# Optimization experiments

Hardware: AMD Instinct MI355X
Metric: run time of the kernel (lower is better)

Reference implementation:

```python
import jax, jax.numpy as jnp
import numpy as np
from jax import lax

B, T, I, H, O = 2048, 512, 1, 64, 1


def setup_inputs() -> dict:
    key = jax.random.key(0)
    ks = jax.random.split(key, 7)
    stdv = 1.0 / np.sqrt(H)
    return {
        "x": jax.random.normal(ks[0], (B, T, I), dtype=jnp.float32),
        "w_ih": jax.random.uniform(ks[1], (4 * H, I), jnp.float32, -stdv, stdv),
        "w_hh": jax.random.uniform(ks[2], (4 * H, H), jnp.float32, -stdv, stdv),
        "b_ih": jax.random.uniform(ks[3], (4 * H,), jnp.float32, -stdv, stdv),
        "b_hh": jax.random.uniform(ks[4], (4 * H,), jnp.float32, -stdv, stdv),
        "w_fc": jax.random.uniform(ks[5], (O, H), jnp.float32, -stdv, stdv),
        "b_fc": jax.random.uniform(ks[6], (O,), jnp.float32, -stdv, stdv),
    }


def reference(x, w_ih, w_hh, b_ih, b_hh, w_fc, b_fc):
    # x: [B, T, I] (batch_first). Precompute input contribution to gates for all t.
    xT = jnp.swapaxes(x, 0, 1)                                  # [T, B, I]
    x_gates = jnp.einsum("tbi,gi->tbg", xT, w_ih) + b_ih + b_hh  # [T, B, 4H]

    def step(carry, xg):
        h, c = carry
        gates = xg + h @ w_hh.T                                  # [B, 4H]
        i, f, g, o = jnp.split(gates, 4, axis=-1)                # PyTorch gate order i,f,g,o
        i = jax.nn.sigmoid(i)
        f = jax.nn.sigmoid(f)
        g = jnp.tanh(g)
        o = jax.nn.sigmoid(o)
        c = f * c + i * g
        h = o * jnp.tanh(c)
        return (h, c), h

    h0 = jnp.zeros((x.shape[0], w_hh.shape[1]), x.dtype)
    c0 = jnp.zeros_like(h0)
    _, hs = lax.scan(step, (h0, c0), x_gates)                    # hs: [T, B, H]
    hs = jnp.swapaxes(hs, 0, 1)                                  # [B, T, H]
    return hs @ w_fc.T + b_fc                                    # [B, T, O]
```

## Files before the change

### kernel.cpp

```cpp
#include <hip/hip_runtime.h>

#define T_STEPS 512
#define HSTR 80
#define XSTRIDE 520
#define OSTRIDE 513
#define NB 4

typedef _Float16 half8v __attribute__((ext_vector_type(8)));
typedef _Float16 half4v __attribute__((ext_vector_type(4)));
typedef float f32x4 __attribute__((ext_vector_type(4)));

#define K1 1.442695041f
#define K2 2.885390082f

__device__ __forceinline__ float ex2(float x) {
#if __has_builtin(__builtin_amdgcn_exp2f)
    return __builtin_amdgcn_exp2f(x);
#else
    return exp2f(x);
#endif
}
__device__ __forceinline__ float rcp_fast(float x) {
#if __has_builtin(__builtin_amdgcn_rcpf)
    return __builtin_amdgcn_rcpf(x);
#else
    return 1.0f / x;
#endif
}

__device__ __forceinline__ float out_dot(half8v a0, half8v a1,
                                         const float* wfc0, const float* wfc1) {
    float s = 0.f;
#pragma unroll
    for (int j = 0; j < 8; ++j) s = fmaf((float)a0[j], wfc0[j], s);
#pragma unroll
    for (int j = 0; j < 8; ++j) s = fmaf((float)a1[j], wfc1[j], s);
    s += __shfl_xor(s, 16);
    s += __shfl_xor(s, 32);
    return s;
}

__global__ __launch_bounds__(256, 2) void lstm_kernel(
    const float* __restrict__ x, const float* __restrict__ w_ih,
    const float* __restrict__ w_hh, const float* __restrict__ b_ih,
    const float* __restrict__ b_hh, const float* __restrict__ w_fc,
    const float* __restrict__ b_fc, float* __restrict__ out)
{
    __shared__ __align__(16) _Float16 hbuf[2][NB * HSTR];
    __shared__ __align__(16) _Float16 xls[NB * XSTRIDE];
    __shared__ __align__(16) float ols[NB * OSTRIDE];

    const int tid  = threadIdx.x;
    const int w    = tid >> 6;
    const int lane = tid & 63;
    const int q    = lane >> 4;
    const int c    = lane & 15;
    const int bown = q;
    const int b0   = blockIdx.x * NB;

    for (int i = tid; i < NB * 128; i += 256) {
        int b  = i >> 7;
        int t4 = i & 127;
        float4 v = *(const float4*)(x + (size_t)(b0 + b) * T_STEPS + t4 * 4);
        half4v hv;
        hv[0] = (_Float16)v.x; hv[1] = (_Float16)v.y;
        hv[2] = (_Float16)v.z; hv[3] = (_Float16)v.w;
        *(half4v*)(&xls[b * XSTRIDE + t4 * 4]) = hv;
    }
    for (int i = tid; i < 2 * NB * HSTR / 2; i += 256) ((int*)hbuf)[i] = 0;

    const float sK[4] = { -K1, -K1, K2, -K1 };
    half8v bfrag[4][2];
    float biasS[4], wihS[4];
#pragma unroll
    for (int n = 0; n < 4; ++n) {
        int g = 64 * n + 16 * w + c;
        biasS[n] = (b_ih[g] + b_hh[g]) * sK[n];
        wihS[n]  = w_ih[g] * sK[n];
#pragma unroll
        for (int kk = 0; kk < 2; ++kk) {
            const float* wp = w_hh + g * 64 + 32 * kk + 8 * q;
            float4 lo  = *(const float4*)(wp);
            float4 hi4 = *(const float4*)(wp + 4);
            half8v f;
            f[0] = (_Float16)(lo.x  * sK[n]); f[1] = (_Float16)(lo.y  * sK[n]);
            f[2] = (_Float16)(lo.z  * sK[n]); f[3] = (_Float16)(lo.w  * sK[n]);
            f[4] = (_Float16)(hi4.x * sK[n]); f[5] = (_Float16)(hi4.y * sK[n]);
            f[6] = (_Float16)(hi4.z * sK[n]); f[7] = (_Float16)(hi4.w * sK[n]);
            bfrag[n][kk] = f;
        }
    }

    float wfc0[8], wfc1[8];
#pragma unroll
    for (int j = 0; j < 8; ++j) { wfc0[j] = w_fc[8 * q + j]; wfc1[j] = w_fc[32 + 8 * q + j]; }
    const float bfc = b_fc[0];

    float cs = 0.f;
    const f32x4 zeroq = {0.f, 0.f, 0.f, 0.f};

    __syncthreads();

    half8v sa0 = {}, sa1 = {};

    for (int tq = 0; tq < 128; ++tq) {
        half4v xh = *(const half4v*)(&xls[bown * XSTRIDE + tq * 4]);

#pragma unroll
        for (int dt = 0; dt < 4; ++dt) {
            const int t  = tq * 4 + dt;
            const int rb = t & 1;
            const _Float16* hrd = hbuf[rb];

            const _Float16* hp = hrd + (c >> 2) * HSTR + 8 * q;
            half8v a0 = *(const half8v*)(hp);
            half8v a1 = *(const half8v*)(hp + 32);

            if (dt == w) { sa0 = a0; sa1 = a1; }

            const float xv = (float)xh[dt];
            float xb[4];
#pragma unroll
            for (int n = 0; n < 4; ++n) xb[n] = fmaf(xv, wihS[n], biasS[n]);

            f32x4 acc[4];
#pragma unroll
            for (int n = 0; n < 4; ++n) {
                acc[n] = __builtin_amdgcn_mfma_f32_16x16x32_f16(a1, bfrag[n][1], zeroq, 0, 0, 0);
                acc[n] = __builtin_amdgcn_mfma_f32_16x16x32_f16(a0, bfrag[n][0], acc[n], 0, 0, 0);
            }

            float v4[4];
#pragma unroll
            for (int n = 0; n < 4; ++n) v4[n] = acc[n][0] + xb[n];

            _Float16* hwr = hbuf[rb ^ 1];
            {
                float A  = ex2(v4[0]);
                float Bt = ex2(v4[2]);
                float ig = (Bt - 1.0f) * rcp_fast((1.0f + A) * (1.0f + Bt));
                float rf = rcp_fast(1.0f + ex2(v4[1]));
                cs = fmaf(cs, rf, ig);
                float cc = fminf(fmaxf(cs, -15.f), 15.f);
                float Ao = ex2(v4[3]);
                float C  = ex2(cc * K2);
                float h  = (C - 1.0f) * rcp_fast((1.0f + Ao) * (1.0f + C));
                hwr[bown * HSTR + 16 * w + c] = (_Float16)h;
            }
            __syncthreads();
        }

        {
            int st = tq * 4 + w;
            if (st > 0) {
                float s = out_dot(sa0, sa1, wfc0, wfc1);
                if (lane < 16 && (lane & 3) == 0)
                    ols[(lane >> 2) * OSTRIDE + (st - 1)] = s + bfc;
            }
        }
    }

    if (w == 3) {
        const _Float16* hp = hbuf[0] + (c >> 2) * HSTR + 8 * q;
        half8v a0 = *(const half8v*)(hp);
        half8v a1 = *(const half8v*)(hp + 32);
        float s = out_dot(a0, a1, wfc0, wfc1);
        if (lane < 16 && (lane & 3) == 0)
            ols[(lane >> 2) * OSTRIDE + (T_STEPS - 1)] = s + bfc;
    }
    __syncthreads();

    for (int i = tid; i < NB * T_STEPS; i += 256) {
        int b = i >> 9;
        int t = i & (T_STEPS - 1);
        out[(size_t)(b0 + b) * T_STEPS + t] = ols[b * OSTRIDE + t];
    }
}

extern "C" void kernel_launch(void* const* d_in, const int* in_sizes, int n_in,
                              void* d_out, int out_size, void* d_ws, size_t ws_size,
                              hipStream_t stream) {
    const float* x    = (const float*)d_in[0];
    const float* w_ih = (const float*)d_in[1];
    const float* w_hh = (const float*)d_in[2];
    const float* b_ih = (const float*)d_in[3];
    const float* b_hh = (const float*)d_in[4];
    const float* w_fc = (const float*)d_in[5];
    const float* b_fc = (const float*)d_in[6];
    float* out = (float*)d_out;
    hipLaunchKernelGGL(lstm_kernel, dim3(2048 / NB), dim3(256), 0, stream,
                       x, w_ih, w_hh, b_ih, b_hh, w_fc, b_fc, out);
}
```

Baseline: 254.7 us.

## Process eight batch rows per block with two independent LSTM chains per wave

Doubles the batch rows per block from 4 to 8. Each wave now runs two independent 4-row groups (A and B) per timestep, each with its own MFMA chains, activations and cell state. This halves the grid to 256 blocks and interleaves two dependency chains to hide MFMA and transcendental latency, at the cost of doubled register and LDS use. Launch bounds drop to one block per SIMD group, so occupancy falls.

New measurement: 324.2 us. 27.3% more time.

```diff
diff --git a/kernel.cpp b/kernel.cpp
--- a/kernel.cpp
+++ b/kernel.cpp
@@ -4,7 +4,7 @@
 #define HSTR 80
 #define XSTRIDE 520
 #define OSTRIDE 513
-#define NB 4
+#define NB 8
 
 typedef _Float16 half8v __attribute__((ext_vector_type(8)));
 typedef _Float16 half4v __attribute__((ext_vector_type(4)));
@@ -28,6 +28,19 @@
 #endif
 }
 
+__device__ __forceinline__ float lstm_act(float v0, float v1, float v2, float v3,
+                                          float& cs) {
+    float A  = ex2(v0);
+    float Bt = ex2(v2);
+    float ig = (Bt - 1.0f) * rcp_fast((1.0f + A) * (1.0f + Bt));
+    float rf = rcp_fast(1.0f + ex2(v1));
+    cs = fmaf(cs, rf, ig);
+    float cc = fminf(fmaxf(cs, -15.f), 15.f);
+    float Ao = ex2(v3);
+    float C  = ex2(cc * K2);
+    return (C - 1.0f) * rcp_fast((1.0f + Ao) * (1.0f + C));
+}
+
 __device__ __forceinline__ float out_dot(half8v a0, half8v a1,
                                          const float* wfc0, const float* wfc1) {
     float s = 0.f;
@@ -40,7 +53,7 @@
     return s;
 }
 
-__global__ __launch_bounds__(256, 2) void lstm_kernel(
+__global__ __launch_bounds__(256, 1) void lstm_kernel(
     const float* __restrict__ x, const float* __restrict__ w_ih,
     const float* __restrict__ w_hh, const float* __restrict__ b_ih,
     const float* __restrict__ b_hh, const float* __restrict__ w_fc,
@@ -55,7 +68,6 @@
     const int lane = tid & 63;
     const int q    = lane >> 4;
     const int c    = lane & 15;
-    const int bown = q;
     const int b0   = blockIdx.x * NB;
 
     for (int i = tid; i < NB * 128; i += 256) {
@@ -96,15 +108,16 @@
     for (int j = 0; j < 8; ++j) { wfc0[j] = w_fc[8 * q + j]; wfc1[j] = w_fc[32 + 8 * q + j]; }
     const float bfc = b_fc[0];
 
-    float cs = 0.f;
+    float csA = 0.f, csB = 0.f;
     const f32x4 zeroq = {0.f, 0.f, 0.f, 0.f};
 
     __syncthreads();
 
-    half8v sa0 = {}, sa1 = {};
+    half8v sa0A = {}, sa1A = {}, sa0B = {}, sa1B = {};
 
     for (int tq = 0; tq < 128; ++tq) {
-        half4v xh = *(const half4v*)(&xls[bown * XSTRIDE + tq * 4]);
+        half4v xhA = *(const half4v*)(&xls[q * XSTRIDE + tq * 4]);
+        half4v xhB = *(const half4v*)(&xls[(4 + q) * XSTRIDE + tq * 4]);
 
 #pragma unroll
         for (int dt = 0; dt < 4; ++dt) {
@@ -112,61 +125,76 @@
             const int rb = t & 1;
             const _Float16* hrd = hbuf[rb];
 
-            const _Float16* hp = hrd + (c >> 2) * HSTR + 8 * q;
-            half8v a0 = *(const half8v*)(hp);
-            half8v a1 = *(const half8v*)(hp + 32);
-
-            if (dt == w) { sa0 = a0; sa1 = a1; }
-
-            const float xv = (float)xh[dt];
-            float xb[4];
-#pragma unroll
-            for (int n = 0; n < 4; ++n) xb[n] = fmaf(xv, wihS[n], biasS[n]);
-
-            f32x4 acc[4];
+            const _Float16* hpA = hrd + (c >> 2) * HSTR + 8 * q;
+            const _Float16* hpB = hrd + (4 + (c >> 2)) * HSTR + 8 * q;
+            half8v a0A = *(const half8v*)(hpA);
+            half8v a1A = *(const half8v*)(hpA + 32);
+            half8v a0B = *(const half8v*)(hpB);
+            half8v a1B = *(const half8v*)(hpB + 32);
+
+            if (dt == w) { sa0A = a0A; sa1A = a1A; sa0B = a0B; sa1B = a1B; }
+
+            const float xvA = (float)xhA[dt], xvB = (float)xhB[dt];
+            float xbA[4], xbB[4];
 #pragma unroll
             for (int n = 0; n < 4; ++n) {
-                acc[n] = __builtin_amdgcn_mfma_f32_16x16x32_f16(a1, bfrag[n][1], zeroq, 0, 0, 0);
-                acc[n] = __builtin_amdgcn_mfma_f32_16x16x32_f16(a0, bfrag[n][0], acc[n], 0, 0, 0);
-            }
-
-            float v4[4];
-#pragma unroll
-            for (int n = 0; n < 4; ++n) v4[n] = acc[n][0] + xb[n];
+                xbA[n] = fmaf(xvA, wihS[n], biasS[n]);
+                xbB[n] = fmaf(xvB, wihS[n], biasS[n]);
+            }
+
+            f32x4 accA[4], accB[4];
+#pragma unroll
+            for (int n = 0; n < 4; ++n) {
+                accA[n] = __builtin_amdgcn_mfma_f32_16x16x32_f16(a1A, bfrag[n][1], zeroq, 0, 0, 0);
+                accA[n] = __builtin_amdgcn_mfma_f32_16x16x32_f16(a0A, bfrag[n][0], accA[n], 0, 0, 0);
+            }
+#pragma unroll
+            for (int n = 0; n < 4; ++n) {
+                accB[n] = __builtin_amdgcn_mfma_f32_16x16x32_f16(a1B, bfrag[n][1], zeroq, 0, 0, 0);
+                accB[n] = __builtin_amdgcn_mfma_f32_16x16x32_f16(a0B, bfrag[n][0], accB[n], 0, 0, 0);
+            }
+
+            float vA[4], vB[4];
+#pragma unroll
+            for (int n = 0; n < 4; ++n) vA[n] = accA[n][0] + xbA[n];
+#pragma unroll
+            for (int n = 0; n < 4; ++n) vB[n] = accB[n][0] + xbB[n];
 
             _Float16* hwr = hbuf[rb ^ 1];
-            {
-                float A  = ex2(v4[0]);
-                float Bt = ex2(v4[2]);
-                float ig = (Bt - 1.0f) * rcp_fast((1.0f + A) * (1.0f + Bt));
-                float rf = rcp_fast(1.0f + ex2(v4[1]));
-                cs = fmaf(cs, rf, ig);
-                float cc = fminf(fmaxf(cs, -15.f), 15.f);
-                float Ao = ex2(v4[3]);
-                float C  = ex2(cc * K2);
-                float h  = (C - 1.0f) * rcp_fast((1.0f + Ao) * (1.0f + C));
-                hwr[bown * HSTR + 16 * w + c] = (_Float16)h;
-            }
+            float hA = lstm_act(vA[0], vA[1], vA[2], vA[3], csA);
+            hwr[q * HSTR + 16 * w + c] = (_Float16)hA;
+            float hB = lstm_act(vB[0], vB[1], vB[2], vB[3], csB);
+            hwr[(4 + q) * HSTR + 16 * w + c] = (_Float16)hB;
+
             __syncthreads();
         }
 
         {
             int st = tq * 4 + w;
             if (st > 0) {
-                float s = out_dot(sa0, sa1, wfc0, wfc1);
-                if (lane < 16 && (lane & 3) == 0)
-                    ols[(lane >> 2) * OSTRIDE + (st - 1)] = s + bfc;
+                float sA = out_dot(sa0A, sa1A, wfc0, wfc1);
+                float sB = out_dot(sa0B, sa1B, wfc0, wfc1);
+                if (lane < 16 && (lane & 3) == 0) {
+                    ols[(lane >> 2) * OSTRIDE + (st - 1)]       = sA + bfc;
+                    ols[(4 + (lane >> 2)) * OSTRIDE + (st - 1)] = sB + bfc;
+                }
             }
         }
     }
 
     if (w == 3) {
-        const _Float16* hp = hbuf[0] + (c >> 2) * HSTR + 8 * q;
-        half8v a0 = *(const half8v*)(hp);
-        half8v a1 = *(const half8v*)(hp + 32);
-        float s = out_dot(a0, a1, wfc0, wfc1);
-        if (lane < 16 && (lane & 3) == 0)
-            ols[(lane >> 2) * OSTRIDE + (T_STEPS - 1)] = s + bfc;
+        const _Float16* hpA = hbuf[0] + (c >> 2) * HSTR + 8 * q;
+        const _Float16* hpB = hbuf[0] + (4 + (c >> 2)) * HSTR + 8 * q;
+        half8v a0A = *(const half8v*)(hpA);
+        half8v a1A = *(const half8v*)(hpA + 32);
+        half8v a0B = *(const half8v*)(hpB);
+        half8v a1B = *(const half8v*)(hpB + 32);
+        float sA = out_dot(a0A, a1A, wfc0, wfc1);
+        float sB = out_dot(a0B, a1B, wfc0, wfc1);
+        if (lane < 16 && (lane & 3) == 0) {
+            ols[(lane >> 2) * OSTRIDE + (T_STEPS - 1)]       = sA + bfc;
+            ols[(4 + (lane >> 2)) * OSTRIDE + (T_STEPS - 1)] = sB + bfc;
+        }
     }
     __syncthreads();
 
```

## Halve LSTM block to two waves, each computing two hidden-unit slices per step

Applied to the files above, without the earlier changes.

Changes the per-block work split from four wavefronts, each owning 16 hidden units, to two wavefronts each owning 32 units in two 16-unit halves with separate MFMA groups and cell states. The goal is cheaper per-step barriers among fewer waves, and interleaving one half's activation math with the other half's matrix ops inside a wave. The cost is twice the serial work per wave on the recurrence critical path, more registers per thread, and fewer resident waves per CU for latency hiding. The output-projection schedule is changed to match the two-wave layout.

Result: slower. 390.7 us (+53.4%).

```diff
diff --git a/kernel.cpp b/kernel.cpp
--- a/kernel.cpp
+++ b/kernel.cpp
@@ -8,6 +8,7 @@
 
 typedef _Float16 half8v __attribute__((ext_vector_type(8)));
 typedef _Float16 half4v __attribute__((ext_vector_type(4)));
+typedef _Float16 half2v __attribute__((ext_vector_type(2)));
 typedef float f32x4 __attribute__((ext_vector_type(4)));
 
 #define K1 1.442695041f
@@ -28,6 +29,19 @@
 #endif
 }
 
+__device__ __forceinline__ float lstm_act(float v0, float v1, float v2, float v3,
+                                          float& cs) {
+    float A  = ex2(v0);
+    float Bt = ex2(v2);
+    float ig = (Bt - 1.0f) * rcp_fast((1.0f + A) * (1.0f + Bt));
+    float rf = rcp_fast(1.0f + ex2(v1));
+    cs = fmaf(cs, rf, ig);
+    float cc = fminf(fmaxf(cs, -15.f), 15.f);
+    float Ao = ex2(v3);
+    float C  = ex2(cc * K2);
+    return (C - 1.0f) * rcp_fast((1.0f + Ao) * (1.0f + C));
+}
+
 __device__ __forceinline__ float out_dot(half8v a0, half8v a1,
                                          const float* wfc0, const float* wfc1) {
     float s = 0.f;
@@ -40,7 +54,7 @@
     return s;
 }
 
-__global__ __launch_bounds__(256, 2) void lstm_kernel(
+__global__ __launch_bounds__(128, 1) void lstm_kernel(
     const float* __restrict__ x, const float* __restrict__ w_ih,
     const float* __restrict__ w_hh, const float* __restrict__ b_ih,
     const float* __restrict__ b_hh, const float* __restrict__ w_fc,
@@ -55,10 +69,9 @@
     const int lane = tid & 63;
     const int q    = lane >> 4;
     const int c    = lane & 15;
-    const int bown = q;
     const int b0   = blockIdx.x * NB;
 
-    for (int i = tid; i < NB * 128; i += 256) {
+    for (int i = tid; i < NB * 128; i += 128) {
         int b  = i >> 7;
         int t4 = i & 127;
         float4 v = *(const float4*)(x + (size_t)(b0 + b) * T_STEPS + t4 * 4);
@@ -67,27 +80,30 @@
         hv[2] = (_Float16)v.z; hv[3] = (_Float16)v.w;
         *(half4v*)(&xls[b * XSTRIDE + t4 * 4]) = hv;
     }
-    for (int i = tid; i < 2 * NB * HSTR / 2; i += 256) ((int*)hbuf)[i] = 0;
+    for (int i = tid; i < 2 * NB * HSTR / 2; i += 128) ((int*)hbuf)[i] = 0;
 
     const float sK[4] = { -K1, -K1, K2, -K1 };
-    half8v bfrag[4][2];
-    float biasS[4], wihS[4];
+    half8v bfrag[4][2][2];
+    float biasS[4][2], wihS[4][2];
 #pragma unroll
     for (int n = 0; n < 4; ++n) {
-        int g = 64 * n + 16 * w + c;
-        biasS[n] = (b_ih[g] + b_hh[g]) * sK[n];
-        wihS[n]  = w_ih[g] * sK[n];
-#pragma unroll
-        for (int kk = 0; kk < 2; ++kk) {
-            const float* wp = w_hh + g * 64 + 32 * kk + 8 * q;
-            float4 lo  = *(const float4*)(wp);
-            float4 hi4 = *(const float4*)(wp + 4);
-            half8v f;
-            f[0] = (_Float16)(lo.x  * sK[n]); f[1] = (_Float16)(lo.y  * sK[n]);
-            f[2] = (_Float16)(lo.z  * sK[n]); f[3] = (_Float16)(lo.w  * sK[n]);
-            f[4] = (_Float16)(hi4.x * sK[n]); f[5] = (_Float16)(hi4.y * sK[n]);
-            f[6] = (_Float16)(hi4.z * sK[n]); f[7] = (_Float16)(hi4.w * sK[n]);
-            bfrag[n][kk] = f;
+#pragma unroll
+        for (int ui = 0; ui < 2; ++ui) {
+            int g = 64 * n + 32 * w + 16 * ui + c;
+            biasS[n][ui] = (b_ih[g] + b_hh[g]) * sK[n];
+            wihS[n][ui]  = w_ih[g] * sK[n];
+#pragma unroll
+            for (int kk = 0; kk < 2; ++kk) {
+                const float* wp = w_hh + g * 64 + 32 * kk + 8 * q;
+                float4 lo  = *(const float4*)(wp);
+                float4 hi4 = *(const float4*)(wp + 4);
+                half8v f;
+                f[0] = (_Float16)(lo.x  * sK[n]); f[1] = (_Float16)(lo.y  * sK[n]);
+                f[2] = (_Float16)(lo.z  * sK[n]); f[3] = (_Float16)(lo.w  * sK[n]);
+                f[4] = (_Float16)(hi4.x * sK[n]); f[5] = (_Float16)(hi4.y * sK[n]);
+                f[6] = (_Float16)(hi4.z * sK[n]); f[7] = (_Float16)(hi4.w * sK[n]);
+                bfrag[n][ui][kk] = f;
+            }
         }
     }
 
@@ -96,62 +112,66 @@
     for (int j = 0; j < 8; ++j) { wfc0[j] = w_fc[8 * q + j]; wfc1[j] = w_fc[32 + 8 * q + j]; }
     const float bfc = b_fc[0];
 
-    float cs = 0.f;
+    float cs0 = 0.f, cs1 = 0.f;
     const f32x4 zeroq = {0.f, 0.f, 0.f, 0.f};
 
     __syncthreads();
 
     half8v sa0 = {}, sa1 = {};
 
-    for (int tq = 0; tq < 128; ++tq) {
-        half4v xh = *(const half4v*)(&xls[bown * XSTRIDE + tq * 4]);
-
-#pragma unroll
-        for (int dt = 0; dt < 4; ++dt) {
-            const int t  = tq * 4 + dt;
+    for (int tq = 0; tq < 256; ++tq) {
+        half2v xh = *(const half2v*)(&xls[q * XSTRIDE + 2 * tq]);
+
+#pragma unroll
+        for (int dt = 0; dt < 2; ++dt) {
+            const int t  = 2 * tq + dt;
             const int rb = t & 1;
-            const _Float16* hrd = hbuf[rb];
-
-            const _Float16* hp = hrd + (c >> 2) * HSTR + 8 * q;
+
+            const _Float16* hp = hbuf[rb] + (c >> 2) * HSTR + 8 * q;
             half8v a0 = *(const half8v*)(hp);
             half8v a1 = *(const half8v*)(hp + 32);
 
             if (dt == w) { sa0 = a0; sa1 = a1; }
 
             const float xv = (float)xh[dt];
-            float xb[4];
-#pragma unroll
-            for (int n = 0; n < 4; ++n) xb[n] = fmaf(xv, wihS[n], biasS[n]);
-
-            f32x4 acc[4];
+            float xb[4][2];
 #pragma unroll
             for (int n = 0; n < 4; ++n) {
-                acc[n] = __builtin_amdgcn_mfma_f32_16x16x32_f16(a1, bfrag[n][1], zeroq, 0, 0, 0);
-                acc[n] = __builtin_amdgcn_mfma_f32_16x16x32_f16(a0, bfrag[n][0], acc[n], 0, 0, 0);
-            }
-
-            float v4[4];
-#pragma unroll
-            for (int n = 0; n < 4; ++n) v4[n] = acc[n][0] + xb[n];
+                xb[n][0] = fmaf(xv, wihS[n][0], biasS[n][0]);
+                xb[n][1] = fmaf(xv, wihS[n][1], biasS[n][1]);
+            }
 
             _Float16* hwr = hbuf[rb ^ 1];
+
+            f32x4 acc0[4];
+#pragma unroll
+            for (int n = 0; n < 4; ++n) {
+                acc0[n] = __builtin_amdgcn_mfma_f32_16x16x32_f16(a1, bfrag[n][0][1], zeroq, 0, 0, 0);
+                acc0[n] = __builtin_amdgcn_mfma_f32_16x16x32_f16(a0, bfrag[n][0][0], acc0[n], 0, 0, 0);
+            }
             {
-                float A  = ex2(v4[0]);
-                float Bt = ex2(v4[2]);
-                float ig = (Bt - 1.0f) * rcp_fast((1.0f + A) * (1.0f + Bt));
-                float rf = rcp_fast(1.0f + ex2(v4[1]));
-                cs = fmaf(cs, rf, ig);
-                float cc = fminf(fmaxf(cs, -15.f), 15.f);
-                float Ao = ex2(v4[3]);
-                float C  = ex2(cc * K2);
-                float h  = (C - 1.0f) * rcp_fast((1.0f + Ao) * (1.0f + C));
-                hwr[bown * HSTR + 16 * w + c] = (_Float16)h;
-            }
+                float h0 = lstm_act(acc0[0][0] + xb[0][0], acc0[1][0] + xb[1][0],
+                                    acc0[2][0] + xb[2][0], acc0[3][0] + xb[3][0], cs0);
+                hwr[q * HSTR + 32 * w + c] = (_Float16)h0;
+            }
+
+            f32x4 acc1[4];
+#pragma unroll
+            for (int n = 0; n < 4; ++n) {
+                acc1[n] = __builtin_amdgcn_mfma_f32_16x16x32_f16(a1, bfrag[n][1][1], zeroq, 0, 0, 0);
+                acc1[n] = __builtin_amdgcn_mfma_f32_16x16x32_f16(a0, bfrag[n][1][0], acc1[n], 0, 0, 0);
+            }
+            {
+                float h1 = lstm_act(acc1[0][0] + xb[0][1], acc1[1][0] + xb[1][1],
+                                    acc1[2][0] + xb[2][1], acc1[3][0] + xb[3][1], cs1);
+                hwr[q * HSTR + 32 * w + 16 + c] = (_Float16)h1;
+            }
+
             __syncthreads();
         }
 
         {
-            int st = tq * 4 + w;
+            int st = 2 * tq + w;
             if (st > 0) {
                 float s = out_dot(sa0, sa1, wfc0, wfc1);
                 if (lane < 16 && (lane & 3) == 0)
@@ -160,7 +180,7 @@
         }
     }
 
-    if (w == 3) {
+    if (w == 1) {
         const _Float16* hp = hbuf[0] + (c >> 2) * HSTR + 8 * q;
         half8v a0 = *(const half8v*)(hp);
         half8v a1 = *(const half8v*)(hp + 32);
@@ -170,7 +190,7 @@
     }
     __syncthreads();
 
-    for (int i = tid; i < NB * T_STEPS; i += 256) {
+    for (int i = tid; i < NB * T_STEPS; i += 128) {
         int b = i >> 9;
         int t = i & (T_STEPS - 1);
         out[(size_t)(b0 + b) * T_STEPS + t] = ols[b * OSTRIDE + t];
@@ -188,6 +208,6 @@
     const float* w_fc = (const float*)d_in[5];
     const float* b_fc = (const float*)d_in[6];
     float* out = (float*)d_out;
-    hipLaunchKernelGGL(lstm_kernel, dim3(2048 / NB), dim3(256), 0, stream,
+    hipLaunchKernelGGL(lstm_kernel, dim3(2048 / NB), dim3(128), 0, stream,
                        x, w_ih, w_hh, b_ih, b_hh, w_fc, b_fc, out);
 }
```

## Give each wavefront its own batch pair and software-pipeline the two hidden halves

Applied to the files above, without the earlier changes.

Each wavefront now owns two batch rows and holds the full recurrent weight matrix in registers, so the per-step block-wide __syncthreads is replaced by wave-local LDS exchange with s_waitcnt. The hidden state is split into two 32-unit halves whose gate activations are staggered against the MFMAs of the other half, with sched_group_barrier hints to interleave transcendental math and matrix ops. The grid drops to 256 blocks with one block per CU, so the goal is to remove barrier latency and hide the activation chain behind MFMA work. The cost is much higher register pressure from holding 32 weight fragments per lane, plus lower occupancy.

Measured after the change: 376.4 us. 1.48x slower.

```diff
diff --git a/kernel.cpp b/kernel.cpp
--- a/kernel.cpp
+++ b/kernel.cpp
@@ -4,7 +4,6 @@
 #define HSTR 80
 #define XSTRIDE 520
 #define OSTRIDE 513
-#define NB 4
 
 typedef _Float16 half8v __attribute__((ext_vector_type(8)));
 typedef _Float16 half4v __attribute__((ext_vector_type(4)));
@@ -12,6 +11,11 @@
 
 #define K1 1.442695041f
 #define K2 2.885390082f
+#define CZCL 43.28085123f
+
+#define MFMA16(A,B,C) __builtin_amdgcn_mfma_f32_16x16x32_f16((A),(B),(C),0,0,0)
+#define SGB(m,n) __builtin_amdgcn_sched_group_barrier((m),(n),0)
+#define LGKM0 asm volatile("s_waitcnt lgkmcnt(0)" ::: "memory")
 
 __device__ __forceinline__ float ex2(float x) {
 #if __has_builtin(__builtin_amdgcn_exp2f)
@@ -28,67 +32,62 @@
 #endif
 }
 
-__device__ __forceinline__ float out_dot(half8v a0, half8v a1,
-                                         const float* wfc0, const float* wfc1) {
-    float s = 0.f;
-#pragma unroll
-    for (int j = 0; j < 8; ++j) s = fmaf((float)a0[j], wfc0[j], s);
-#pragma unroll
-    for (int j = 0; j < 8; ++j) s = fmaf((float)a1[j], wfc1[j], s);
-    s += __shfl_xor(s, 16);
-    s += __shfl_xor(s, 32);
-    return s;
-}
-
-__global__ __launch_bounds__(256, 2) void lstm_kernel(
+__global__ __launch_bounds__(256, 1) void lstm_kernel(
     const float* __restrict__ x, const float* __restrict__ w_ih,
     const float* __restrict__ w_hh, const float* __restrict__ b_ih,
     const float* __restrict__ b_hh, const float* __restrict__ w_fc,
     const float* __restrict__ b_fc, float* __restrict__ out)
 {
-    __shared__ __align__(16) _Float16 hbuf[2][NB * HSTR];
-    __shared__ __align__(16) _Float16 xls[NB * XSTRIDE];
-    __shared__ __align__(16) float ols[NB * OSTRIDE];
+    __shared__ __align__(16) _Float16 hls[4][2 * HSTR];
+    __shared__ __align__(16) _Float16 xls[8][XSTRIDE];
+    __shared__ __align__(16) float    ols[8][OSTRIDE];
 
     const int tid  = threadIdx.x;
     const int w    = tid >> 6;
     const int lane = tid & 63;
     const int q    = lane >> 4;
     const int c    = lane & 15;
-    const int bown = q;
-    const int b0   = blockIdx.x * NB;
-
-    for (int i = tid; i < NB * 128; i += 256) {
-        int b  = i >> 7;
-        int t4 = i & 127;
-        float4 v = *(const float4*)(x + (size_t)(b0 + b) * T_STEPS + t4 * 4);
+    const int up   = q & 1;
+    const int mb   = q >> 1;
+    const int bw   = blockIdx.x * 8 + 2 * w;
+
+    for (int i = lane; i < 256; i += 64) {
+        int r = i >> 7, t4 = i & 127;
+        float4 v = *(const float4*)(x + (size_t)(bw + r) * T_STEPS + t4 * 4);
         half4v hv;
         hv[0] = (_Float16)v.x; hv[1] = (_Float16)v.y;
         hv[2] = (_Float16)v.z; hv[3] = (_Float16)v.w;
-        *(half4v*)(&xls[b * XSTRIDE + t4 * 4]) = hv;
-    }
-    for (int i = tid; i < 2 * NB * HSTR / 2; i += 256) ((int*)hbuf)[i] = 0;
+        *(half4v*)(&xls[2 * w + r][t4 * 4]) = hv;
+    }
+    _Float16* hbw = &hls[w][0];
+    for (int i = lane; i < 80; i += 64) ((int*)hbw)[i] = 0;
 
     const float sK[4] = { -K1, -K1, K2, -K1 };
-    half8v bfrag[4][2];
-    float biasS[4], wihS[4];
+    half8v bfrag[4][4][2];
+    float biasA[4], wihA[4], biasB[4], wihB[4];
 #pragma unroll
     for (int n = 0; n < 4; ++n) {
-        int g = 64 * n + 16 * w + c;
-        biasS[n] = (b_ih[g] + b_hh[g]) * sK[n];
-        wihS[n]  = w_ih[g] * sK[n];
-#pragma unroll
-        for (int kk = 0; kk < 2; ++kk) {
-            const float* wp = w_hh + g * 64 + 32 * kk + 8 * q;
-            float4 lo  = *(const float4*)(wp);
-            float4 hi4 = *(const float4*)(wp + 4);
-            half8v f;
-            f[0] = (_Float16)(lo.x  * sK[n]); f[1] = (_Float16)(lo.y  * sK[n]);
-            f[2] = (_Float16)(lo.z  * sK[n]); f[3] = (_Float16)(lo.w  * sK[n]);
-            f[4] = (_Float16)(hi4.x * sK[n]); f[5] = (_Float16)(hi4.y * sK[n]);
-            f[6] = (_Float16)(hi4.z * sK[n]); f[7] = (_Float16)(hi4.w * sK[n]);
-            bfrag[n][kk] = f;
+#pragma unroll
+        for (int u = 0; u < 4; ++u) {
+            int g = 64 * n + 16 * u + c;
+#pragma unroll
+            for (int kk = 0; kk < 2; ++kk) {
+                const float* wp = w_hh + g * 64 + 32 * kk + 8 * q;
+                float4 lo  = *(const float4*)(wp);
+                float4 hi4 = *(const float4*)(wp + 4);
+                half8v f;
+                f[0] = (_Float16)(lo.x  * sK[n]); f[1] = (_Float16)(lo.y  * sK[n]);
+                f[2] = (_Float16)(lo.z  * sK[n]); f[3] = (_Float16)(lo.w  * sK[n]);
+                f[4] = (_Float16)(hi4.x * sK[n]); f[5] = (_Float16)(hi4.y * sK[n]);
+                f[6] = (_Float16)(hi4.z * sK[n]); f[7] = (_Float16)(hi4.w * sK[n]);
+                bfrag[n][u][kk] = f;
+            }
         }
+        int gA = 64 * n + 16 * up + c;
+        biasA[n] = (b_ih[gA] + b_hh[gA]) * sK[n];
+        wihA[n]  = w_ih[gA] * sK[n];
+        biasB[n] = (b_ih[gA + 32] + b_hh[gA + 32]) * sK[n];
+        wihB[n]  = w_ih[gA + 32] * sK[n];
     }
 
     float wfc0[8], wfc1[8];
@@ -96,84 +95,141 @@
     for (int j = 0; j < 8; ++j) { wfc0[j] = w_fc[8 * q + j]; wfc1[j] = w_fc[32 + 8 * q + j]; }
     const float bfc = b_fc[0];
 
-    float cs = 0.f;
+    float czA = 0.f, czB = 0.f;
+    float vB0 = 100.f, vB1 = 100.f, vB2 = 0.f, vB3 = 100.f;
     const f32x4 zeroq = {0.f, 0.f, 0.f, 0.f};
 
-    __syncthreads();
-
-    half8v sa0 = {}, sa1 = {};
+    LGKM0;
+    const _Float16* hp = hbw + (c >> 3) * HSTR + 8 * q;
+    half8v a0 = *(const half8v*)(hp);
+    half8v a1 = *(const half8v*)(hp + 32);
+
+    f32x4 acc[4][4];
 
     for (int tq = 0; tq < 128; ++tq) {
-        half4v xh = *(const half4v*)(&xls[bown * XSTRIDE + tq * 4]);
-
+        half4v xh = *(const half4v*)(&xls[2 * w + mb][tq * 4]);
 #pragma unroll
         for (int dt = 0; dt < 4; ++dt) {
             const int t  = tq * 4 + dt;
-            const int rb = t & 1;
-            const _Float16* hrd = hbuf[rb];
-
-            const _Float16* hp = hrd + (c >> 2) * HSTR + 8 * q;
-            half8v a0 = *(const half8v*)(hp);
-            half8v a1 = *(const half8v*)(hp + 32);
-
-            if (dt == w) { sa0 = a0; sa1 = a1; }
-
             const float xv = (float)xh[dt];
-            float xb[4];
-#pragma unroll
-            for (int n = 0; n < 4; ++n) xb[n] = fmaf(xv, wihS[n], biasS[n]);
-
-            f32x4 acc[4];
-#pragma unroll
-            for (int n = 0; n < 4; ++n) {
-                acc[n] = __builtin_amdgcn_mfma_f32_16x16x32_f16(a1, bfrag[n][1], zeroq, 0, 0, 0);
-                acc[n] = __builtin_amdgcn_mfma_f32_16x16x32_f16(a0, bfrag[n][0], acc[n], 0, 0, 0);
-            }
-
-            float v4[4];
-#pragma unroll
-            for (int n = 0; n < 4; ++n) v4[n] = acc[n][0] + xb[n];
-
-            _Float16* hwr = hbuf[rb ^ 1];
-            {
-                float A  = ex2(v4[0]);
-                float Bt = ex2(v4[2]);
-                float ig = (Bt - 1.0f) * rcp_fast((1.0f + A) * (1.0f + Bt));
-                float rf = rcp_fast(1.0f + ex2(v4[1]));
-                cs = fmaf(cs, rf, ig);
-                float cc = fminf(fmaxf(cs, -15.f), 15.f);
-                float Ao = ex2(v4[3]);
-                float C  = ex2(cc * K2);
-                float h  = (C - 1.0f) * rcp_fast((1.0f + Ao) * (1.0f + C));
-                hwr[bown * HSTR + 16 * w + c] = (_Float16)h;
-            }
-            __syncthreads();
+
+            acc[0][0] = MFMA16(a0, bfrag[0][0][0], zeroq);
+            acc[1][0] = MFMA16(a0, bfrag[1][0][0], zeroq);
+            float bA = ex2(vB0), bB = ex2(vB2), bF = ex2(vB1), bO = ex2(vB3);
+            SGB(8, 2); SGB(2, 4);
+            acc[2][0] = MFMA16(a0, bfrag[2][0][0], zeroq);
+            acc[3][0] = MFMA16(a0, bfrag[3][0][0], zeroq);
+            float bR  = rcp_fast((1.f + bA) * (1.f + bB));
+            float bpg = fmaf(bB, K2, -K2);
+            float brf = rcp_fast(1.f + bF);
+            SGB(8, 2); SGB(2, 6);
+            acc[0][1] = MFMA16(a0, bfrag[0][1][0], zeroq);
+            acc[1][1] = MFMA16(a0, bfrag[1][1][0], zeroq);
+            czB = fmaf(czB, brf, bpg * bR);
+            float bcc = fminf(fmaxf(czB, -CZCL), CZCL);
+            float bC  = ex2(bcc);
+            SGB(8, 2); SGB(2, 5);
+            acc[2][1] = MFMA16(a0, bfrag[2][1][0], zeroq);
+            acc[3][1] = MFMA16(a0, bfrag[3][1][0], zeroq);
+            float bh = (bC - 1.f) * rcp_fast((1.f + bO) * (1.f + bC));
+            hbw[mb * HSTR + 32 + 16 * up + c] = (_Float16)bh;
+            SGB(8, 2); SGB(2, 6);
+            LGKM0;
+            a1 = *(const half8v*)(hp + 32);
+            acc[0][2] = MFMA16(a0, bfrag[0][2][0], zeroq);
+            acc[1][2] = MFMA16(a0, bfrag[1][2][0], zeroq);
+            acc[2][2] = MFMA16(a0, bfrag[2][2][0], zeroq);
+            acc[3][2] = MFMA16(a0, bfrag[3][2][0], zeroq);
+            acc[0][3] = MFMA16(a0, bfrag[0][3][0], zeroq);
+            acc[1][3] = MFMA16(a0, bfrag[1][3][0], zeroq);
+            acc[2][3] = MFMA16(a0, bfrag[2][3][0], zeroq);
+            acc[3][3] = MFMA16(a0, bfrag[3][3][0], zeroq);
+            SGB(8, 8);
+
+            acc[0][0] = MFMA16(a1, bfrag[0][0][1], acc[0][0]);
+            acc[1][0] = MFMA16(a1, bfrag[1][0][1], acc[1][0]);
+            acc[2][0] = MFMA16(a1, bfrag[2][0][1], acc[2][0]);
+            acc[3][0] = MFMA16(a1, bfrag[3][0][1], acc[3][0]);
+            acc[0][1] = MFMA16(a1, bfrag[0][1][1], acc[0][1]);
+            acc[1][1] = MFMA16(a1, bfrag[1][1][1], acc[1][1]);
+            acc[2][1] = MFMA16(a1, bfrag[2][1][1], acc[2][1]);
+            acc[3][1] = MFMA16(a1, bfrag[3][1][1], acc[3][1]);
+            SGB(8, 8);
+            float av0 = (up ? acc[0][1][0] : acc[0][0][0]) + fmaf(xv, wihA[0], biasA[0]);
+            float av1 = (up ? acc[1][1][0] : acc[1][0][0]) + fmaf(xv, wihA[1], biasA[1]);
+            float av2 = (up ? acc[2][1][0] : acc[2][0][0]) + fmaf(xv, wihA[2], biasA[2]);
+            float av3 = (up ? acc[3][1][0] : acc[3][0][0]) + fmaf(xv, wihA[3], biasA[3]);
+            float aA = ex2(av0), aB2 = ex2(av2), aF = ex2(av1), aO = ex2(av3);
+            SGB(2, 16);
+            acc[0][2] = MFMA16(a1, bfrag[0][2][1], acc[0][2]);
+            acc[1][2] = MFMA16(a1, bfrag[1][2][1], acc[1][2]);
+            float aR  = rcp_fast((1.f + aA) * (1.f + aB2));
+            float apg = fmaf(aB2, K2, -K2);
+            float arf = rcp_fast(1.f + aF);
+            SGB(8, 2); SGB(2, 6);
+            acc[2][2] = MFMA16(a1, bfrag[2][2][1], acc[2][2]);
+            acc[3][2] = MFMA16(a1, bfrag[3][2][1], acc[3][2]);
+            czA = fmaf(czA, arf, apg * aR);
+            float acl = fminf(fmaxf(czA, -CZCL), CZCL);
+            float aC  = ex2(acl);
+            SGB(8, 2); SGB(2, 5);
+            acc[0][3] = MFMA16(a1, bfrag[0][3][1], acc[0][3]);
+            acc[1][3] = MFMA16(a1, bfrag[1][3][1], acc[1][3]);
+            float ah = (aC - 1.f) * rcp_fast((1.f + aO) * (1.f + aC));
+            hbw[mb * HSTR + 16 * up + c] = (_Float16)ah;
+            SGB(8, 2); SGB(2, 6);
+            LGKM0;
+            half8v a0n = *(const half8v*)(hp);
+            acc[2][3] = MFMA16(a1, bfrag[2][3][1], acc[2][3]);
+            acc[3][3] = MFMA16(a1, bfrag[3][3][1], acc[3][3]);
+            SGB(8, 2);
+
+            float s = 0.f;
+#pragma unroll
+            for (int j = 0; j < 8; ++j) s = fmaf((float)a0[j], wfc0[j], s);
+#pragma unroll
+            for (int j = 0; j < 8; ++j) s = fmaf((float)a1[j], wfc1[j], s);
+            s += __shfl_xor(s, 16);
+            s += __shfl_xor(s, 32);
+            if (t && (lane == 0 || lane == 8))
+                ols[2 * w + (lane >> 3)][t - 1] = s + bfc;
+
+            vB0 = (up ? acc[0][3][0] : acc[0][2][0]) + fmaf(xv, wihB[0], biasB[0]);
+            vB1 = (up ? acc[1][3][0] : acc[1][2][0]) + fmaf(xv, wihB[1], biasB[1]);
+            vB2 = (up ? acc[2][3][0] : acc[2][2][0]) + fmaf(xv, wihB[2], biasB[2]);
+            vB3 = (up ? acc[3][3][0] : acc[3][2][0]) + fmaf(xv, wihB[3], biasB[3]);
+
+            a0 = a0n;
         }
-
-        {
-            int st = tq * 4 + w;
-            if (st > 0) {
-                float s = out_dot(sa0, sa1, wfc0, wfc1);
-                if (lane < 16 && (lane & 3) == 0)
-                    ols[(lane >> 2) * OSTRIDE + (st - 1)] = s + bfc;
-            }
-        }
-    }
-
-    if (w == 3) {
-        const _Float16* hp = hbuf[0] + (c >> 2) * HSTR + 8 * q;
-        half8v a0 = *(const half8v*)(hp);
-        half8v a1 = *(const half8v*)(hp + 32);
-        float s = out_dot(a0, a1, wfc0, wfc1);
-        if (lane < 16 && (lane & 3) == 0)
-            ols[(lane >> 2) * OSTRIDE + (T_STEPS - 1)] = s + bfc;
-    }
-    __syncthreads();
-
-    for (int i = tid; i < NB * T_STEPS; i += 256) {
-        int b = i >> 9;
-        int t = i & (T_STEPS - 1);
-        out[(size_t)(b0 + b) * T_STEPS + t] = ols[b * OSTRIDE + t];
+    }
+
+    {
+        float bA = ex2(vB0), bB = ex2(vB2), bF = ex2(vB1), bO = ex2(vB3);
+        float bR  = rcp_fast((1.f + bA) * (1.f + bB));
+        float bpg = fmaf(bB, K2, -K2);
+        float brf = rcp_fast(1.f + bF);
+        czB = fmaf(czB, brf, bpg * bR);
+        float bcc = fminf(fmaxf(czB, -CZCL), CZCL);
+        float bC  = ex2(bcc);
+        float bh = (bC - 1.f) * rcp_fast((1.f + bO) * (1.f + bC));
+        hbw[mb * HSTR + 32 + 16 * up + c] = (_Float16)bh;
+        LGKM0;
+        a1 = *(const half8v*)(hp + 32);
+        float s = 0.f;
+#pragma unroll
+        for (int j = 0; j < 8; ++j) s = fmaf((float)a0[j], wfc0[j], s);
+#pragma unroll
+        for (int j = 0; j < 8; ++j) s = fmaf((float)a1[j], wfc1[j], s);
+        s += __shfl_xor(s, 16);
+        s += __shfl_xor(s, 32);
+        if (lane == 0 || lane == 8)
+            ols[2 * w + (lane >> 3)][T_STEPS - 1] = s + bfc;
+    }
+    LGKM0;
+
+    for (int i = lane; i < 2 * T_STEPS; i += 64) {
+        int r = i >> 9, tt = i & (T_STEPS - 1);
+        out[(size_t)(bw + r) * T_STEPS + tt] = ols[2 * w + r][tt];
     }
 }
 
@@ -188,6 +244,6 @@
     const float* w_fc = (const float*)d_in[5];
     const float* b_fc = (const float*)d_in[6];
     float* out = (float*)d_out;
-    hipLaunchKernelGGL(lstm_kernel, dim3(2048 / NB), dim3(256), 0, stream,
+    hipLaunchKernelGGL(lstm_kernel, dim3(256), dim3(256), 0, stream,
                        x, w_ih, w_hh, b_ih, b_hh, w_fc, b_fc, out);
 }
```
